# Kernel tuning notes

Hardware: AMD Instinct MI355X
Metric: run time of the kernel (lower is better)

Reference implementation:

```python
import jax, jax.numpy as jnp
import numpy as np

D_MODEL = 1024
N_HEADS = 16
D_HEAD = 64
SEQ = 2048
BATCH = 2
ATTN_SCALE = float(np.sqrt(D_HEAD))  # cfg.use_attn_scale = True
NEG_INF = -1e9


def setup_inputs() -> dict:
    key = jax.random.key(0)
    ks = jax.random.split(key, 8)
    s = 0.02
    return {
        "query_input": jax.random.normal(ks[0], (BATCH, SEQ, D_MODEL), jnp.float32),
        "key_input": jax.random.normal(ks[1], (BATCH, SEQ, D_MODEL), jnp.float32),
        "value_input": jax.random.normal(ks[2], (BATCH, SEQ, D_MODEL), jnp.float32),
        "W_Q": jax.random.normal(ks[3], (N_HEADS, D_MODEL, D_HEAD), jnp.float32) * s,
        "W_K": jax.random.normal(ks[4], (N_HEADS, D_MODEL, D_HEAD), jnp.float32) * s,
        "W_V": jax.random.normal(ks[5], (N_HEADS, D_MODEL, D_HEAD), jnp.float32) * s,
        "W_O": jax.random.normal(ks[6], (N_HEADS, D_HEAD, D_MODEL), jnp.float32) * s,
        "b_Q": jnp.zeros((N_HEADS, D_HEAD), jnp.float32),
        "b_K": jnp.zeros((N_HEADS, D_HEAD), jnp.float32),
        "b_V": jnp.zeros((N_HEADS, D_HEAD), jnp.float32),
        "b_O": jnp.zeros((D_MODEL,), jnp.float32),
    }


def reference(query_input, key_input, value_input, W_Q, W_K, W_V, W_O, b_Q, b_K, b_V, b_O):
    # QKV projections: [batch, pos, d_model] x [head, d_model, d_head] -> [batch, pos, head, d_head]
    q = jnp.einsum("bpd,hde->bphe", query_input, W_Q) + b_Q
    k = jnp.einsum("bpd,hde->bphe", key_input, W_K) + b_K
    v = jnp.einsum("bpd,hde->bphe", value_input, W_V) + b_V

    # attn scores [batch, head, query_pos, key_pos]
    scores = jnp.einsum("bqhe,bkhe->bhqk", q, k) / ATTN_SCALE

    # causal mask (attn_type == 'global'): tril over [n_ctx, n_ctx] sliced to seq
    causal = jnp.tril(jnp.ones((SEQ, SEQ), bool))
    scores = jnp.where(causal[None, None, :, :], scores, NEG_INF)

    pattern = jax.nn.softmax(scores, axis=-1)

    # z: [batch, query_pos, head, d_head]
    z = jnp.einsum("bhqk,bkhe->bqhe", pattern, v)

    # output projection: [batch, pos, d_model]
    out = jnp.einsum("bqhe,hed->bqd", z, W_O) + b_O
    return out
```

## Files before the change

### kernel.cpp

```cpp
#include <hip/hip_runtime.h>
#include <stdint.h>


typedef __attribute__((ext_vector_type(8))) short short8;
typedef __attribute__((ext_vector_type(4))) float floatx4;
typedef __attribute__((ext_vector_type(4))) unsigned int uintx4;

#define MFMA16(a, b, c) __builtin_amdgcn_mfma_f32_16x16x32_bf16(a, b, c, 0, 0, 0)

__device__ __forceinline__ unsigned short f2b(float f) {
  unsigned int u = __builtin_bit_cast(unsigned int, f);
  u = (u + 0x7fffu + ((u >> 16) & 1u)) >> 16;
  return (unsigned short)u;
}
__device__ __forceinline__ float exp2f_fast(float x) {
#if __has_builtin(__builtin_amdgcn_exp2f)
  return __builtin_amdgcn_exp2f(x);
#else
  return exp2f(x);
#endif
}
__device__ __forceinline__ unsigned int pack2_bf16(float lo, float hi) {
#if __has_builtin(__builtin_amdgcn_perm)
  return __builtin_amdgcn_perm(__builtin_bit_cast(unsigned int, hi),
                               __builtin_bit_cast(unsigned int, lo), 0x07060302u);
#else
  return (__builtin_bit_cast(unsigned int, lo) >> 16) |
         (__builtin_bit_cast(unsigned int, hi) & 0xffff0000u);
#endif
}

__device__ __forceinline__ void async_copy16(void* lds, const void* g) {
  __builtin_amdgcn_global_load_lds(
      (const __attribute__((address_space(1))) unsigned int*)g,
      (__attribute__((address_space(3))) unsigned int*)lds, 16, 0, 0);
}

__global__ __launch_bounds__(256) void conv_x3(const float* __restrict__ a,
                                               const float* __restrict__ b,
                                               const float* __restrict__ c,
                                               unsigned short* __restrict__ out) {
  const float* in = (blockIdx.y == 0) ? a : ((blockIdx.y == 1) ? b : c);
  size_t i = (size_t)blockIdx.x * 256 + threadIdx.x;
  float4 v = ((const float4*)in)[i];
  ushort4 u;
  u.x = f2b(v.x); u.y = f2b(v.y); u.z = f2b(v.z); u.w = f2b(v.w);
  ((ushort4*)(out + (size_t)blockIdx.y * 4194304))[i] = u;
}

__global__ __launch_bounds__(256) void conv_w3(const float* __restrict__ a,
                                               const float* __restrict__ b,
                                               const float* __restrict__ c,
                                               unsigned short* __restrict__ out) {
  __shared__ float T[64][65];
  const float* in = (blockIdx.y == 0) ? a : ((blockIdx.y == 1) ? b : c);
  const int t = threadIdx.x, rr = t >> 4, cc = t & 15;
  const int h = blockIdx.x >> 4, d0 = (blockIdx.x & 15) << 6;
#pragma unroll
  for (int it = 0; it < 4; ++it) {
    int dl = it * 16 + rr;
    float4 v = *(const float4*)&in[(size_t)h * 65536 + (size_t)(d0 + dl) * 64 + cc * 4];
    T[dl][cc * 4 + 0] = v.x; T[dl][cc * 4 + 1] = v.y;
    T[dl][cc * 4 + 2] = v.z; T[dl][cc * 4 + 3] = v.w;
  }
  __syncthreads();
  unsigned short* ob = out + (size_t)blockIdx.y * 1048576;
#pragma unroll
  for (int it = 0; it < 4; ++it) {
    int e = it * 16 + rr;
    ushort4 u;
    u.x = f2b(T[cc * 4 + 0][e]); u.y = f2b(T[cc * 4 + 1][e]);
    u.z = f2b(T[cc * 4 + 2][e]); u.w = f2b(T[cc * 4 + 3][e]);
    *(ushort4*)&ob[(size_t)(h * 64 + e) * 1024 + d0 + cc * 4] = u;
  }
}

__global__ __launch_bounds__(256) void conv_wo(const float* __restrict__ in,
                                               unsigned short* __restrict__ out) {
  __shared__ float T[64][65];
  const int t = threadIdx.x, rr = t >> 4, cc = t & 15;
  const int r0 = (blockIdx.x & 15) << 6;
  const int c0 = (blockIdx.x >> 4) << 6;
#pragma unroll
  for (int it = 0; it < 4; ++it) {
    int rl = it * 16 + rr;
    float4 v = *(const float4*)&in[(size_t)(r0 + rl) * 1024 + c0 + cc * 4];
    T[rl][cc * 4 + 0] = v.x; T[rl][cc * 4 + 1] = v.y;
    T[rl][cc * 4 + 2] = v.z; T[rl][cc * 4 + 3] = v.w;
  }
  __syncthreads();
#pragma unroll
  for (int it = 0; it < 4; ++it) {
    int dl = it * 16 + rr;
    ushort4 u;
    u.x = f2b(T[cc * 4 + 0][dl]); u.y = f2b(T[cc * 4 + 1][dl]);
    u.z = f2b(T[cc * 4 + 2][dl]); u.w = f2b(T[cc * 4 + 3][dl]);
    *(ushort4*)&out[(size_t)(c0 + dl) * 1024 + r0 + cc * 4] = u;
  }
}

__global__ __launch_bounds__(256) void gemm128(
    const short* __restrict__ A0, const short* __restrict__ A1,
    const short* __restrict__ A2, const short* __restrict__ B0,
    const short* __restrict__ B1, const short* __restrict__ B2,
    const float* __restrict__ bias0, const float* __restrict__ bias1,
    const float* __restrict__ bias2, unsigned short* __restrict__ ob0,
    unsigned short* __restrict__ ob1, unsigned short* __restrict__ ob2,
    float* __restrict__ outf, int qkv, float qscale) {
  __shared__ short As[128 * 32];
  __shared__ short Bs[128 * 32];

  const int z = blockIdx.z;
  const short* A = (z == 0) ? A0 : (z == 1) ? A1 : A2;
  const short* Bt = (z == 0) ? B0 : (z == 1) ? B1 : B2;

  const int tid = threadIdx.x;
  const int lane = tid & 63, w = tid >> 6;
  const int quad = lane >> 4, col = lane & 15;
  const int m0 = blockIdx.y * 128, n0 = blockIdx.x * 128;
  const int wm = (w >> 1) * 64, wn = (w & 1) * 64;

  floatx4 acc[4][4] = {};

  const int lr = lane >> 2, gc = (lane & 3) ^ ((lane >> 3) & 3);
  const short* ga = A + (size_t)(m0 + w * 32 + lr) * 1024 + gc * 8;
  const short* gb = Bt + (size_t)(n0 + w * 32 + lr) * 1024 + gc * 8;
  short* la = &As[(w * 32) * 32];
  short* lb = &Bs[(w * 32) * 32];
  const int asw = (col >> 1) & 3;

  for (int k0 = 0; k0 < 1024; k0 += 32) {
    async_copy16(la, ga);
    async_copy16(la + 16 * 32, ga + 16 * 1024);
    async_copy16(lb, gb);
    async_copy16(lb + 16 * 32, gb + 16 * 1024);
    ga += 32; gb += 32;
    __syncthreads();
    short8 af[4], bf[4];
#pragma unroll
    for (int mi = 0; mi < 4; ++mi)
      af[mi] = *(const short8*)&As[(wm + mi * 16 + col) * 32 + ((quad ^ asw) * 8)];
#pragma unroll
    for (int nj = 0; nj < 4; ++nj)
      bf[nj] = *(const short8*)&Bs[(wn + nj * 16 + col) * 32 + ((quad ^ asw) * 8)];
#pragma unroll
    for (int mi = 0; mi < 4; ++mi)
#pragma unroll
      for (int nj = 0; nj < 4; ++nj)
        acc[mi][nj] = MFMA16(af[mi], bf[nj], acc[mi][nj]);
    __syncthreads();
  }

  const float* bias = (z == 0) ? bias0 : (z == 1) ? bias1 : bias2;
  unsigned short* outb = (z == 0) ? ob0 : (z == 1) ? ob1 : ob2;
  const int mode = qkv ? ((z == 2) ? 2 : 1) : 0;
  const float scale = (qkv && z == 0) ? qscale : 1.0f;

  float bv[4];
#pragma unroll
  for (int nj = 0; nj < 4; ++nj) bv[nj] = bias[n0 + wn + nj * 16 + col];

#pragma unroll
  for (int mi = 0; mi < 4; ++mi)
#pragma unroll
    for (int nj = 0; nj < 4; ++nj)
#pragma unroll
      for (int r = 0; r < 4; ++r) {
        int m = m0 + wm + mi * 16 + quad * 4 + r;
        int n = n0 + wn + nj * 16 + col;
        float v = acc[mi][nj][r] + bv[nj];
        if (mode == 0) {
          outf[(size_t)m * 1024 + n] = v;
        } else {
          v *= scale;
          unsigned short hv = f2b(v);
          int bb = m >> 11, s = m & 2047, h = n >> 6, e = n & 63;
          size_t addr;
          if (mode == 1)
            addr = (((size_t)bb * 16 + h) * 2048 + s) * 64 + e;
          else
            addr = (((size_t)bb * 16 + h) * 64 + e) * 2048 + s;
          outb[addr] = hv;
        }
      }
}

__device__ __forceinline__ void exchange4(const unsigned int* u01,
                                          const unsigned int* u23, int srcA,
                                          int srcB, bool hiq, short8& pf0,
                                          short8& pf1) {
  unsigned int xA0 = (unsigned int)__shfl((int)u01[0], srcA, 64);
  unsigned int xA1 = (unsigned int)__shfl((int)u01[1], srcA, 64);
  unsigned int yA0 = (unsigned int)__shfl((int)u23[0], srcA, 64);
  unsigned int yA1 = (unsigned int)__shfl((int)u23[1], srcA, 64);
  unsigned int xB0 = (unsigned int)__shfl((int)u01[0], srcB, 64);
  unsigned int xB1 = (unsigned int)__shfl((int)u01[1], srcB, 64);
  unsigned int yB0 = (unsigned int)__shfl((int)u23[0], srcB, 64);
  unsigned int yB1 = (unsigned int)__shfl((int)u23[1], srcB, 64);
  uintx4 v0;
  v0.x = hiq ? xA1 : xA0; v0.y = hiq ? yA1 : yA0;
  v0.z = hiq ? xB1 : xB0; v0.w = hiq ? yB1 : yB0;
  pf0 = __builtin_bit_cast(short8, v0);
  xA0 = (unsigned int)__shfl((int)u01[2], srcA, 64);
  xA1 = (unsigned int)__shfl((int)u01[3], srcA, 64);
  yA0 = (unsigned int)__shfl((int)u23[2], srcA, 64);
  yA1 = (unsigned int)__shfl((int)u23[3], srcA, 64);
  xB0 = (unsigned int)__shfl((int)u01[2], srcB, 64);
  xB1 = (unsigned int)__shfl((int)u01[3], srcB, 64);
  yB0 = (unsigned int)__shfl((int)u23[2], srcB, 64);
  yB1 = (unsigned int)__shfl((int)u23[3], srcB, 64);
  uintx4 v1;
  v1.x = hiq ? xA1 : xA0; v1.y = hiq ? yA1 : yA0;
  v1.z = hiq ? xB1 : xB0; v1.w = hiq ? yB1 : yB0;
  pf1 = __builtin_bit_cast(short8, v1);
}

__global__ __launch_bounds__(256) void attn(const short* __restrict__ q,
                                            const short* __restrict__ k,
                                            const short* __restrict__ vt,
                                            unsigned short* __restrict__ z) {
  __shared__ short Ks[64 * 64];
  __shared__ short Vs[64 * 64];

  const int tid = threadIdx.x;
  const int lane = tid & 63, w = tid >> 6;
  const int quad = lane >> 4, col = lane & 15;
  const int qt = 15 - (blockIdx.x >> 5), bh = blockIdx.x & 31;
  const int q0 = qt * 128, qw0 = q0 + w * 32;
  const size_t base = (size_t)bh * (2048 * 64);

  short8 bq[2][2];
#pragma unroll
  for (int h = 0; h < 2; ++h) {
    const short* qp = q + base + (size_t)(qw0 + h * 16 + col) * 64 + quad * 8;
    bq[h][0] = *(const short8*)qp;
    bq[h][1] = *(const short8*)(qp + 32);
  }

  floatx4 o[2][4] = {};
  float m_run[2] = {-1e30f, -1e30f}, l_run[2] = {0.f, 0.f};

  const short* kg = k + base;
  const short* vg = vt + base;
  const int ksw = col & 7;
  const int slr = lane >> 3, sgc = (lane & 7) ^ slr;
  const int srcA = ((quad & 1) << 5) + col, srcB = srcA + 16;
  const bool hiq = (quad & 2) != 0;
  const int qlw = w * 32 + col;
  const int ntiles = 2 * qt + 2;

  for (int t = 0; t < ntiles; ++t) {
    const int kv0 = t * 64;
    {
      const short* kr = kg + (size_t)(kv0 + w * 16 + slr) * 64 + sgc * 8;
      async_copy16(&Ks[(w * 16) * 64], kr);
      async_copy16(&Ks[(w * 16 + 8) * 64], kr + 8 * 64);
      const short* vr = vg + (size_t)(w * 16 + slr) * 2048 + kv0 + sgc * 8;
      async_copy16(&Vs[(w * 16) * 64], vr);
      async_copy16(&Vs[(w * 16 + 8) * 64], vr + 8 * 2048);
    }
    __syncthreads();

    const int dbase = kv0 - q0;
    const bool diag = (dbase >= 0);
    const int mtneed = diag ? ((32 * w + 31 - dbase) >> 4) : 3;

    if (mtneed >= 0) {
      const int mmax = (mtneed > 3) ? 3 : mtneed;

      floatx4 st[2][4];
#pragma unroll
      for (int mt = 0; mt < 4; ++mt) {
        if (mt <= mmax) {
          const short* kb = &Ks[(mt * 16 + col) * 64];
          short8 ka0 = *(const short8*)(kb + (quad ^ ksw) * 8);
          short8 ka1 = *(const short8*)(kb + ((quad + 4) ^ ksw) * 8);
#pragma unroll
          for (int h = 0; h < 2; ++h) {
            floatx4 a = {0.f, 0.f, 0.f, 0.f};
            a = MFMA16(ka0, bq[h][0], a);
            a = MFMA16(ka1, bq[h][1], a);
            if (diag) {
              const int kl = dbase + mt * 16 + quad * 4;
              const int ql = qlw + h * 16;
#pragma unroll
              for (int r = 0; r < 4; ++r)
                if (kl + r > ql) a[r] = -1e9f;
            }
            st[h][mt] = a;
          }
        }
      }

      float alpha[2];
      unsigned int u01[2][4], u23[2][4];
#pragma unroll
      for (int h = 0; h < 2; ++h) {
        float pmax = -3e38f;
#pragma unroll
        for (int mt = 0; mt < 4; ++mt)
          if (mt <= mmax) {
#pragma unroll
            for (int r = 0; r < 4; ++r) pmax = fmaxf(pmax, st[h][mt][r]);
          }
        pmax = fmaxf(pmax, __shfl_xor(pmax, 16, 64));
        pmax = fmaxf(pmax, __shfl_xor(pmax, 32, 64));
        float mnew = fmaxf(m_run[h], pmax);
        alpha[h] = exp2f_fast(m_run[h] - mnew);
        m_run[h] = mnew;
        float lsum = 0.f;
#pragma unroll
        for (int mt = 0; mt < 4; ++mt) {
          if (mt <= mmax) {
            float p0 = exp2f_fast(st[h][mt][0] - mnew);
            float p1 = exp2f_fast(st[h][mt][1] - mnew);
            float p2 = exp2f_fast(st[h][mt][2] - mnew);
            float p3 = exp2f_fast(st[h][mt][3] - mnew);
            lsum += (p0 + p1) + (p2 + p3);
            u01[h][mt] = pack2_bf16(p0, p1);
            u23[h][mt] = pack2_bf16(p2, p3);
          } else {
            u01[h][mt] = 0u; u23[h][mt] = 0u;
          }
        }
        lsum += __shfl_xor(lsum, 16, 64);
        lsum += __shfl_xor(lsum, 32, 64);
        l_run[h] = l_run[h] * alpha[h] + lsum;
      }

      short8 pf0[2], pf1[2];
#pragma unroll
      for (int h = 0; h < 2; ++h)
        exchange4(u01[h], u23[h], srcA, srcB, hiq, pf0[h], pf1[h]);

#pragma unroll
      for (int et = 0; et < 4; ++et) {
        const short* vb = &Vs[(et * 16 + col) * 64];
        short8 va0 = *(const short8*)(vb + (quad ^ ksw) * 8);
        short8 va1 = *(const short8*)(vb + ((quad + 4) ^ ksw) * 8);
#pragma unroll
        for (int h = 0; h < 2; ++h) {
          floatx4 t0 = o[h][et];
#pragma unroll
          for (int r = 0; r < 4; ++r) t0[r] *= alpha[h];
          t0 = MFMA16(va0, pf0[h], t0);
          t0 = MFMA16(va1, pf1[h], t0);
          o[h][et] = t0;
        }
      }
    }
    __syncthreads();
  }

  const int bb = bh >> 4, hh = bh & 15;
#pragma unroll
  for (int h = 0; h < 2; ++h) {
#if __has_builtin(__builtin_amdgcn_rcpf)
    const float invl = __builtin_amdgcn_rcpf(l_run[h]);
#else
    const float invl = 1.f / l_run[h];
#endif
    unsigned short* zr =
        z + (((size_t)bb * 2048 + qw0 + h * 16 + col) * 16 + hh) * 64;
#pragma unroll
    for (int et = 0; et < 4; ++et) {
      ushort4 u;
      u.x = f2b(o[h][et][0] * invl); u.y = f2b(o[h][et][1] * invl);
      u.z = f2b(o[h][et][2] * invl); u.w = f2b(o[h][et][3] * invl);
      *(ushort4*)&zr[et * 16 + quad * 4] = u;
    }
  }
}

extern "C" void kernel_launch(void* const* d_in, const int* in_sizes, int n_in,
                              void* d_out, int out_size, void* d_ws, size_t ws_size,
                              hipStream_t stream) {
  (void)in_sizes; (void)n_in; (void)out_size; (void)ws_size;
  const float* Xq = (const float*)d_in[0];
  const float* Xk = (const float*)d_in[1];
  const float* Xv = (const float*)d_in[2];
  const float* WQ = (const float*)d_in[3];
  const float* WK = (const float*)d_in[4];
  const float* WV = (const float*)d_in[5];
  const float* WO = (const float*)d_in[6];
  const float* bQ = (const float*)d_in[7];
  const float* bK = (const float*)d_in[8];
  const float* bV = (const float*)d_in[9];
  const float* bO = (const float*)d_in[10];
  float* out = (float*)d_out;

  unsigned short* xqb = (unsigned short*)d_ws;
  unsigned short* xkb = xqb + 4194304;
  unsigned short* xvb = xkb + 4194304;
  unsigned short* wqt = xvb + 4194304;
  unsigned short* wkt = wqt + 1048576;
  unsigned short* wvt = wkt + 1048576;
  unsigned short* wot = wvt + 1048576;
  unsigned short* qb = wot + 1048576;
  unsigned short* kb = qb + 4194304;
  unsigned short* vtb = kb + 4194304;
  unsigned short* zb = vtb + 4194304;

  conv_x3<<<dim3(4096, 3), 256, 0, stream>>>(Xq, Xk, Xv, xqb);
  conv_w3<<<dim3(256, 3), 256, 0, stream>>>(WQ, WK, WV, wqt);
  conv_wo<<<256, 256, 0, stream>>>(WO, wot);

  const float qscale = 0.125f * 1.44269504088896f;
  gemm128<<<dim3(8, 32, 3), 256, 0, stream>>>(
      (const short*)xqb, (const short*)xkb, (const short*)xvb,
      (const short*)wqt, (const short*)wkt, (const short*)wvt, bQ, bK, bV, qb,
      kb, vtb, nullptr, 1, qscale);

  attn<<<512, 256, 0, stream>>>((const short*)qb, (const short*)kb,
                                (const short*)vtb, zb);

  gemm128<<<dim3(8, 32, 1), 256, 0, stream>>>(
      (const short*)zb, (const short*)zb, (const short*)zb, (const short*)wot,
      (const short*)wot, (const short*)wot, bO, bO, bO, nullptr, nullptr,
      nullptr, out, 0, 1.0f);
}
```

Measured before the change: 258.3 us.

## Halve attention query tile and vectorize GEMM epilogue stores via lane transpose

The attention kernel now gives each block 64 queries instead of 128, with one 16-row query slab per wave, so the launch grows to 1024 blocks and the diagonal masking becomes simpler. This is meant to improve load balance and occupancy across the causal triangle, at the cost of loading each K/V tile into shared memory twice as often. The GEMM epilogue also moves from scalar stores to vector stores: accumulators are transposed within groups of four lanes using shuffles for the Q/K and fp32 outputs, and V^T is written directly as ushort4.

```diff
diff --git a/kernel.cpp b/kernel.cpp
--- a/kernel.cpp
+++ b/kernel.cpp
@@ -34,6 +34,23 @@
   __builtin_amdgcn_global_load_lds(
       (const __attribute__((address_space(1))) unsigned int*)g,
       (__attribute__((address_space(3))) unsigned int*)lds, 16, 0, 0);
+}
+
+__device__ __forceinline__ void xpose4(floatx4& v, int lane) {
+  {
+    float s0 = __shfl_xor(v[1], 1, 64);
+    float s1 = __shfl_xor(v[0], 1, 64);
+    float s2 = __shfl_xor(v[3], 1, 64);
+    float s3 = __shfl_xor(v[2], 1, 64);
+    if (lane & 1) { v[0] = s0; v[2] = s2; } else { v[1] = s1; v[3] = s3; }
+  }
+  {
+    float s0 = __shfl_xor(v[2], 2, 64);
+    float s1 = __shfl_xor(v[3], 2, 64);
+    float s2 = __shfl_xor(v[0], 2, 64);
+    float s3 = __shfl_xor(v[1], 2, 64);
+    if (lane & 2) { v[0] = s0; v[1] = s1; } else { v[2] = s2; v[3] = s3; }
+  }
 }
 
 __global__ __launch_bounds__(256) void conv_x3(const float* __restrict__ a,
@@ -160,29 +177,42 @@
 #pragma unroll
   for (int nj = 0; nj < 4; ++nj) bv[nj] = bias[n0 + wn + nj * 16 + col];
 
-#pragma unroll
-  for (int mi = 0; mi < 4; ++mi)
-#pragma unroll
-    for (int nj = 0; nj < 4; ++nj)
-#pragma unroll
-      for (int r = 0; r < 4; ++r) {
-        int m = m0 + wm + mi * 16 + quad * 4 + r;
+  if (mode == 2) {
+#pragma unroll
+    for (int mi = 0; mi < 4; ++mi)
+#pragma unroll
+      for (int nj = 0; nj < 4; ++nj) {
+        int m = m0 + wm + mi * 16 + quad * 4;
         int n = n0 + wn + nj * 16 + col;
-        float v = acc[mi][nj][r] + bv[nj];
+        int bb = m >> 11, s = m & 2047, h = n >> 6, e = n & 63;
+        ushort4 u;
+        u.x = f2b(acc[mi][nj][0] + bv[nj]);
+        u.y = f2b(acc[mi][nj][1] + bv[nj]);
+        u.z = f2b(acc[mi][nj][2] + bv[nj]);
+        u.w = f2b(acc[mi][nj][3] + bv[nj]);
+        *(ushort4*)&outb[(((size_t)bb * 16 + h) * 64 + e) * 2048 + s] = u;
+      }
+  } else {
+#pragma unroll
+    for (int mi = 0; mi < 4; ++mi)
+#pragma unroll
+      for (int nj = 0; nj < 4; ++nj) {
+        floatx4 v;
+#pragma unroll
+        for (int r = 0; r < 4; ++r) v[r] = (acc[mi][nj][r] + bv[nj]) * scale;
+        xpose4(v, lane);
+        int m = m0 + wm + mi * 16 + quad * 4 + (col & 3);
+        int nb = n0 + wn + nj * 16 + (col & ~3);
         if (mode == 0) {
-          outf[(size_t)m * 1024 + n] = v;
+          *(floatx4*)&outf[(size_t)m * 1024 + nb] = v;
         } else {
-          v *= scale;
-          unsigned short hv = f2b(v);
-          int bb = m >> 11, s = m & 2047, h = n >> 6, e = n & 63;
-          size_t addr;
-          if (mode == 1)
-            addr = (((size_t)bb * 16 + h) * 2048 + s) * 64 + e;
-          else
-            addr = (((size_t)bb * 16 + h) * 64 + e) * 2048 + s;
-          outb[addr] = hv;
+          int bb = m >> 11, s = m & 2047, h = nb >> 6, e = nb & 63;
+          ushort4 u;
+          u.x = f2b(v[0]); u.y = f2b(v[1]); u.z = f2b(v[2]); u.w = f2b(v[3]);
+          *(ushort4*)&outb[(((size_t)bb * 16 + h) * 2048 + s) * 64 + e] = u;
         }
       }
+  }
 }
 
 __device__ __forceinline__ void exchange4(const unsigned int* u01,
@@ -225,20 +255,16 @@
   const int tid = threadIdx.x;
   const int lane = tid & 63, w = tid >> 6;
   const int quad = lane >> 4, col = lane & 15;
-  const int qt = 15 - (blockIdx.x >> 5), bh = blockIdx.x & 31;
-  const int q0 = qt * 128, qw0 = q0 + w * 32;
+  const int qt = 31 - (blockIdx.x >> 5), bh = blockIdx.x & 31;
+  const int q0 = qt * 64, qw0 = q0 + w * 16;
   const size_t base = (size_t)bh * (2048 * 64);
 
-  short8 bq[2][2];
-#pragma unroll
-  for (int h = 0; h < 2; ++h) {
-    const short* qp = q + base + (size_t)(qw0 + h * 16 + col) * 64 + quad * 8;
-    bq[h][0] = *(const short8*)qp;
-    bq[h][1] = *(const short8*)(qp + 32);
-  }
-
-  floatx4 o[2][4] = {};
-  float m_run[2] = {-1e30f, -1e30f}, l_run[2] = {0.f, 0.f};
+  const short* qp = q + base + (size_t)(qw0 + col) * 64 + quad * 8;
+  short8 bq0 = *(const short8*)qp;
+  short8 bq1 = *(const short8*)(qp + 32);
+
+  floatx4 o[4] = {};
+  float m_run = -1e30f, l_run = 0.f;
 
   const short* kg = k + base;
   const short* vg = vt + base;
@@ -246,10 +272,8 @@
   const int slr = lane >> 3, sgc = (lane & 7) ^ slr;
   const int srcA = ((quad & 1) << 5) + col, srcB = srcA + 16;
   const bool hiq = (quad & 2) != 0;
-  const int qlw = w * 32 + col;
-  const int ntiles = 2 * qt + 2;
-
-  for (int t = 0; t < ntiles; ++t) {
+
+  for (int t = 0; t <= qt; ++t) {
     const int kv0 = t * 64;
     {
       const short* kr = kg + (size_t)(kv0 + w * 16 + slr) * 64 + sgc * 8;
@@ -261,114 +285,92 @@
     }
     __syncthreads();
 
-    const int dbase = kv0 - q0;
-    const bool diag = (dbase >= 0);
-    const int mtneed = diag ? ((32 * w + 31 - dbase) >> 4) : 3;
-
-    if (mtneed >= 0) {
-      const int mmax = (mtneed > 3) ? 3 : mtneed;
-
-      floatx4 st[2][4];
-#pragma unroll
-      for (int mt = 0; mt < 4; ++mt) {
-        if (mt <= mmax) {
-          const short* kb = &Ks[(mt * 16 + col) * 64];
-          short8 ka0 = *(const short8*)(kb + (quad ^ ksw) * 8);
-          short8 ka1 = *(const short8*)(kb + ((quad + 4) ^ ksw) * 8);
-#pragma unroll
-          for (int h = 0; h < 2; ++h) {
-            floatx4 a = {0.f, 0.f, 0.f, 0.f};
-            a = MFMA16(ka0, bq[h][0], a);
-            a = MFMA16(ka1, bq[h][1], a);
-            if (diag) {
-              const int kl = dbase + mt * 16 + quad * 4;
-              const int ql = qlw + h * 16;
-#pragma unroll
-              for (int r = 0; r < 4; ++r)
-                if (kl + r > ql) a[r] = -1e9f;
-            }
-            st[h][mt] = a;
-          }
+    const bool diag = (t == qt);
+    const int mtmax = diag ? w : 3;
+
+    floatx4 st[4];
+#pragma unroll
+    for (int mt = 0; mt < 4; ++mt) {
+      if (mt <= mtmax) {
+        const short* kb = &Ks[(mt * 16 + col) * 64];
+        short8 ka0 = *(const short8*)(kb + (quad ^ ksw) * 8);
+        short8 ka1 = *(const short8*)(kb + ((quad + 4) ^ ksw) * 8);
+        floatx4 a = {0.f, 0.f, 0.f, 0.f};
+        a = MFMA16(ka0, bq0, a);
+        a = MFMA16(ka1, bq1, a);
+        if (diag && mt == mtmax) {
+#pragma unroll
+          for (int r = 0; r < 4; ++r)
+            if (quad * 4 + r > col) a[r] = -1e9f;
         }
-      }
-
-      float alpha[2];
-      unsigned int u01[2][4], u23[2][4];
-#pragma unroll
-      for (int h = 0; h < 2; ++h) {
-        float pmax = -3e38f;
-#pragma unroll
-        for (int mt = 0; mt < 4; ++mt)
-          if (mt <= mmax) {
-#pragma unroll
-            for (int r = 0; r < 4; ++r) pmax = fmaxf(pmax, st[h][mt][r]);
-          }
-        pmax = fmaxf(pmax, __shfl_xor(pmax, 16, 64));
-        pmax = fmaxf(pmax, __shfl_xor(pmax, 32, 64));
-        float mnew = fmaxf(m_run[h], pmax);
-        alpha[h] = exp2f_fast(m_run[h] - mnew);
-        m_run[h] = mnew;
-        float lsum = 0.f;
-#pragma unroll
-        for (int mt = 0; mt < 4; ++mt) {
-          if (mt <= mmax) {
-            float p0 = exp2f_fast(st[h][mt][0] - mnew);
-            float p1 = exp2f_fast(st[h][mt][1] - mnew);
-            float p2 = exp2f_fast(st[h][mt][2] - mnew);
-            float p3 = exp2f_fast(st[h][mt][3] - mnew);
-            lsum += (p0 + p1) + (p2 + p3);
-            u01[h][mt] = pack2_bf16(p0, p1);
-            u23[h][mt] = pack2_bf16(p2, p3);
-          } else {
-            u01[h][mt] = 0u; u23[h][mt] = 0u;
-          }
-        }
-        lsum += __shfl_xor(lsum, 16, 64);
-        lsum += __shfl_xor(lsum, 32, 64);
-        l_run[h] = l_run[h] * alpha[h] + lsum;
-      }
-
-      short8 pf0[2], pf1[2];
-#pragma unroll
-      for (int h = 0; h < 2; ++h)
-        exchange4(u01[h], u23[h], srcA, srcB, hiq, pf0[h], pf1[h]);
-
-#pragma unroll
-      for (int et = 0; et < 4; ++et) {
-        const short* vb = &Vs[(et * 16 + col) * 64];
-        short8 va0 = *(const short8*)(vb + (quad ^ ksw) * 8);
-        short8 va1 = *(const short8*)(vb + ((quad + 4) ^ ksw) * 8);
-#pragma unroll
-        for (int h = 0; h < 2; ++h) {
-          floatx4 t0 = o[h][et];
-#pragma unroll
-          for (int r = 0; r < 4; ++r) t0[r] *= alpha[h];
-          t0 = MFMA16(va0, pf0[h], t0);
-          t0 = MFMA16(va1, pf1[h], t0);
-          o[h][et] = t0;
-        }
+        st[mt] = a;
       }
     }
+
+    float pmax = -3e38f;
+#pragma unroll
+    for (int mt = 0; mt < 4; ++mt)
+      if (mt <= mtmax) {
+#pragma unroll
+        for (int r = 0; r < 4; ++r) pmax = fmaxf(pmax, st[mt][r]);
+      }
+    pmax = fmaxf(pmax, __shfl_xor(pmax, 16, 64));
+    pmax = fmaxf(pmax, __shfl_xor(pmax, 32, 64));
+    float mnew = fmaxf(m_run, pmax);
+    float alpha = exp2f_fast(m_run - mnew);
+    m_run = mnew;
+
+    unsigned int u01[4], u23[4];
+    float lsum = 0.f;
+#pragma unroll
+    for (int mt = 0; mt < 4; ++mt) {
+      if (mt <= mtmax) {
+        float p0 = exp2f_fast(st[mt][0] - mnew);
+        float p1 = exp2f_fast(st[mt][1] - mnew);
+        float p2 = exp2f_fast(st[mt][2] - mnew);
+        float p3 = exp2f_fast(st[mt][3] - mnew);
+        lsum += (p0 + p1) + (p2 + p3);
+        u01[mt] = pack2_bf16(p0, p1);
+        u23[mt] = pack2_bf16(p2, p3);
+      } else {
+        u01[mt] = 0u; u23[mt] = 0u;
+      }
+    }
+    lsum += __shfl_xor(lsum, 16, 64);
+    lsum += __shfl_xor(lsum, 32, 64);
+    l_run = l_run * alpha + lsum;
+
+    short8 pf0, pf1;
+    exchange4(u01, u23, srcA, srcB, hiq, pf0, pf1);
+
+#pragma unroll
+    for (int et = 0; et < 4; ++et) {
+      const short* vb = &Vs[(et * 16 + col) * 64];
+      short8 va0 = *(const short8*)(vb + (quad ^ ksw) * 8);
+      short8 va1 = *(const short8*)(vb + ((quad + 4) ^ ksw) * 8);
+      floatx4 t0 = o[et];
+#pragma unroll
+      for (int r = 0; r < 4; ++r) t0[r] *= alpha;
+      t0 = MFMA16(va0, pf0, t0);
+      t0 = MFMA16(va1, pf1, t0);
+      o[et] = t0;
+    }
     __syncthreads();
   }
 
-  const int bb = bh >> 4, hh = bh & 15;
-#pragma unroll
-  for (int h = 0; h < 2; ++h) {
+  const int b = bh >> 4, h = bh & 15;
 #if __has_builtin(__builtin_amdgcn_rcpf)
-    const float invl = __builtin_amdgcn_rcpf(l_run[h]);
+  const float invl = __builtin_amdgcn_rcpf(l_run);
 #else
-    const float invl = 1.f / l_run[h];
+  const float invl = 1.f / l_run;
 #endif
-    unsigned short* zr =
-        z + (((size_t)bb * 2048 + qw0 + h * 16 + col) * 16 + hh) * 64;
-#pragma unroll
-    for (int et = 0; et < 4; ++et) {
-      ushort4 u;
-      u.x = f2b(o[h][et][0] * invl); u.y = f2b(o[h][et][1] * invl);
-      u.z = f2b(o[h][et][2] * invl); u.w = f2b(o[h][et][3] * invl);
-      *(ushort4*)&zr[et * 16 + quad * 4] = u;
-    }
+  unsigned short* zr = z + (((size_t)b * 2048 + qw0 + col) * 16 + h) * 64;
+#pragma unroll
+  for (int et = 0; et < 4; ++et) {
+    ushort4 u;
+    u.x = f2b(o[et][0] * invl); u.y = f2b(o[et][1] * invl);
+    u.z = f2b(o[et][2] * invl); u.w = f2b(o[et][3] * invl);
+    *(ushort4*)&zr[et * 16 + quad * 4] = u;
   }
 }
 
@@ -411,8 +413,8 @@
       (const short*)wqt, (const short*)wkt, (const short*)wvt, bQ, bK, bV, qb,
       kb, vtb, nullptr, 1, qscale);
 
-  attn<<<512, 256, 0, stream>>>((const short*)qb, (const short*)kb,
-                                (const short*)vtb, zb);
+  attn<<<1024, 256, 0, stream>>>((const short*)qb, (const short*)kb,
+                                 (const short*)vtb, zb);
 
   gemm128<<<dim3(8, 32, 1), 256, 0, stream>>>(
       (const short*)zb, (const short*)zb, (const short*)zb, (const short*)wot,
```

Measured after the change: 245.2 us. 5.1% less time.
